# Performance work log

Measured on AMD Instinct MI355X. Metric: run time of the kernel, lower is better.

Reference implementation:

```python
import jax, jax.numpy as jnp
import numpy as np

N = 4096
IN_F = 256
OUT_F = 64
HEADS = 8
ALPHA = 0.2  # LeakyReLU negative slope


def setup_inputs() -> dict:
    key = jax.random.key(0)
    k1, k2, k3, k4 = jax.random.split(key, 4)
    X = jax.random.normal(k1, (N, IN_F), dtype=jnp.float32)
    adj = jax.random.randint(k2, (N, N), 0, 2, dtype=jnp.int32)
    # self-loops so every row has at least one neighbor (softmax well-defined)
    idx = jnp.arange(N)
    adj = adj.at[idx, idx].set(1)
    W = jax.random.normal(k3, (HEADS, IN_F, OUT_F), dtype=jnp.float32) * 0.05
    a = jax.random.normal(k4, (HEADS, 2 * OUT_F, 1), dtype=jnp.float32) * 0.05
    return {"X": X, "adj": adj, "W": W, "a": a}


def reference(X, adj, W, a):
    # H: [heads, N, F]
    H = jnp.einsum('ni,hio->hno', X, W)
    F_ = H.shape[-1]
    # cat([h_i, h_j]) @ a  ==  h_i @ a[:F] + h_j @ a[F:]
    a1 = a[:, :F_, 0]   # [heads, F]
    a2 = a[:, F_:, 0]   # [heads, F]
    f1 = jnp.einsum('hnf,hf->hn', H, a1)  # score contribution of row node i
    f2 = jnp.einsum('hnf,hf->hn', H, a2)  # score contribution of col node j
    e = jax.nn.leaky_relu(f1[:, :, None] + f2[:, None, :], negative_slope=ALPHA)  # [heads, N, N]
    e = jnp.where(adj[None, :, :] == 0, -jnp.inf, e)
    attention = jax.nn.softmax(e, axis=-1)
    # dropout omitted (eval mode)
    H_out = jnp.einsum('hnm,hmf->hnf', attention, H)  # [heads, N, F]
    return H_out.mean(axis=0)  # [N, F]
```

## Files before the change

kernel.cpp:

```cpp
#include <hip/hip_runtime.h>
#include <hip/hip_bf16.h>

#define N_NODES 4096
#define IN_F 256
#define OUT_F 64
#define HEADS 8
#define ALPHA 0.2f

typedef _Float16 f16x8 __attribute__((ext_vector_type(8)));
typedef float f32x4 __attribute__((ext_vector_type(4)));
union U4 { uint4 u; f16x8 h; unsigned w[4]; };

#define WFRAG_OFF 0
#define BFRAG_OFF (WFRAG_OFF + 8*8*4*64*8*2)
#define F1_OFF    (BFRAG_OFF + 8*128*4*64*8*2)
#define GP_OFF    (F1_OFF + 8*4096*4)
#define GN_OFF    (GP_OFF + 8*4096*2)
#define ADJ_OFF   (GN_OFF + 8*4096*2)

static __device__ __forceinline__ unsigned pkmul(unsigned a, unsigned b) {
  unsigned r; asm("v_pk_mul_f16 %0, %1, %2" : "=v"(r) : "v"(a), "v"(b)); return r;
}
static __device__ __forceinline__ unsigned pkmax(unsigned a, unsigned b) {
  unsigned r; asm("v_pk_max_f16 %0, %1, %2" : "=v"(r) : "v"(a), "v"(b)); return r;
}
static __device__ __forceinline__ unsigned short f2h_bits(float f) {
  return __builtin_bit_cast(unsigned short, (_Float16)f);
}

__global__ __launch_bounds__(256) void k_pre(const float* __restrict__ W,
                                             _Float16* __restrict__ wfrag,
                                             float* __restrict__ out) {
  int b = blockIdx.x, t = threadIdx.x;
  if (b < 8) {
    int h = b;
    for (int pos = t; pos < 2048; pos += 256) {
      int kt = pos >> 8, ct = (pos >> 6) & 3, l = pos & 63;
      int lr = l & 15, lg = l >> 4;
#pragma unroll
      for (int e = 0; e < 8; ++e)
        wfrag[(size_t)(((h*8 + kt)*4 + ct)*64 + l) * 8 + e]
          = (_Float16)W[(size_t)(h*256 + kt*32 + lg*8 + e) * 64 + ct*16 + lr];
    }
  } else {
    float4* oz = ((float4*)out) + (size_t)(b - 8) * 8192;
    float4 zz = make_float4(0.f, 0.f, 0.f, 0.f);
    for (int q = t; q < 8192; q += 256) oz[q] = zz;
  }
}

__global__ __launch_bounds__(256) void k_main(
    const float* __restrict__ X, const int* __restrict__ adj,
    const _Float16* __restrict__ wfrag, const float* __restrict__ a,
    unsigned long long* __restrict__ bits, _Float16* __restrict__ bfrag,
    float* __restrict__ f1, _Float16* __restrict__ Gp, _Float16* __restrict__ Gn) {
  int b = blockIdx.x, t = threadIdx.x;
  if (b >= 512) {
    int b2 = b - 512;
    int lane = t & 63;
    int waveid = b2 * 4 + (t >> 6);
#pragma unroll
    for (int it2 = 0; it2 < 8; ++it2) {
      int w0 = waveid + (it2*4 + 0) * 8192;
      int w1 = waveid + (it2*4 + 1) * 8192;
      int w2 = waveid + (it2*4 + 2) * 8192;
      int w3 = waveid + (it2*4 + 3) * 8192;
      int v0 = __builtin_nontemporal_load(adj + (size_t)w0 * 64 + lane);
      int v1 = __builtin_nontemporal_load(adj + (size_t)w1 * 64 + lane);
      int v2 = __builtin_nontemporal_load(adj + (size_t)w2 * 64 + lane);
      int v3 = __builtin_nontemporal_load(adj + (size_t)w3 * 64 + lane);
      unsigned long long m0 = __ballot(v0 != 0);
      unsigned long long m1 = __ballot(v1 != 0);
      unsigned long long m2 = __ballot(v2 != 0);
      unsigned long long m3 = __ballot(v3 != 0);
      if (lane == 0) { bits[w0] = m0; bits[w1] = m1; bits[w2] = m2; bits[w3] = m3; }
    }
    return;
  }
  int h = b & 7, rb = b >> 3;
  int w = t >> 6, l = t & 63;
  int i0 = rb * 64 + w * 16;
  int r = l & 15, g = l >> 4;
  const U4* wv = (const U4*)wfrag;
  f32x4 z = {0.f, 0.f, 0.f, 0.f};
  f32x4 acc[4] = {z, z, z, z};
#pragma unroll
  for (int kt = 0; kt < 8; ++kt) {
    const float4* xr = (const float4*)(X + (size_t)(i0 + r) * 256 + (kt*4 + g) * 8);
    float4 x0 = xr[0], x1 = xr[1];
    U4 af;
    af.h[0] = (_Float16)x0.x; af.h[1] = (_Float16)x0.y;
    af.h[2] = (_Float16)x0.z; af.h[3] = (_Float16)x0.w;
    af.h[4] = (_Float16)x1.x; af.h[5] = (_Float16)x1.y;
    af.h[6] = (_Float16)x1.z; af.h[7] = (_Float16)x1.w;
#pragma unroll
    for (int ct = 0; ct < 4; ++ct) {
      U4 bv = wv[((h*8 + kt)*4 + ct)*64 + l];
      acc[ct] = __builtin_amdgcn_mfma_f32_16x16x32_f16(af.h, bv.h, acc[ct], 0, 0, 0);
    }
  }
  int jb = i0 + g*4;
#pragma unroll
  for (int ct = 0; ct < 4; ++ct) {
    size_t base = ((((size_t)h*128 + (jb>>5))*4 + ct)*64 + ((jb>>3)&3)*16 + r) * 8
                  + (jb & 7);
    union { short4 s; _Float16 hh[4]; } sv;
#pragma unroll
    for (int ri = 0; ri < 4; ++ri) sv.hh[ri] = (_Float16)acc[ct][ri];
    *(short4*)(bfrag + base) = sv.s;
  }
  float a1v[4], a2v[4];
#pragma unroll
  for (int ct = 0; ct < 4; ++ct) {
    a1v[ct] = a[h*128 + ct*16 + r];
    a2v[ct] = a[h*128 + 64 + ct*16 + r];
  }
#pragma unroll
  for (int ri = 0; ri < 4; ++ri) {
    float s1 = acc[0][ri]*a1v[0] + acc[1][ri]*a1v[1]
             + acc[2][ri]*a1v[2] + acc[3][ri]*a1v[3];
    float s2 = acc[0][ri]*a2v[0] + acc[1][ri]*a2v[1]
             + acc[2][ri]*a2v[2] + acc[3][ri]*a2v[3];
#pragma unroll
    for (int off = 1; off < 16; off <<= 1) {
      s1 += __shfl_xor(s1, off);
      s2 += __shfl_xor(s2, off);
    }
    if (r == 0) {
      int row = i0 + g*4 + ri;
      f1[h*4096 + row] = s1;
      Gp[h*4096 + row] = (_Float16)__expf(s2);
      Gn[h*4096 + row] = (_Float16)__expf(ALPHA * s2);
    }
  }
}

#define ATTN_BODY(PF, JT, DOPF) {                                              \
  U4 gp, gn;                                                                   \
  gp.u = Gs0[(JT)*4 + g].u;                                                    \
  gn.u = Gs1[(JT)*4 + g].u;                                                    \
  U4 b0, b1, b2, b3;                                                           \
  b0.u = PF[0]; b1.u = PF[1]; b2.u = PF[2]; b3.u = PF[3];                      \
  _Pragma("unroll")                                                            \
  for (int rg = 0; rg < 2; ++rg) {                                             \
    unsigned wm = Lb[rh32 + rg*16 + r][JT];                                    \
    U4 av;                                                                     \
    _Pragma("unroll")                                                          \
    for (int p = 0; p < 4; ++p) {                                              \
      unsigned pm = pkmax(pkmul(Epp[rg], gp.w[p]), pkmul(Enn[rg], gn.w[p]));   \
      av.w[p] = pm & MLUT[(wm >> (g8 + 2*p)) & 3u];                            \
    }                                                                          \
    acc[rg][0] = __builtin_amdgcn_mfma_f32_16x16x32_f16(av.h, b0.h, acc[rg][0], 0,0,0); \
    acc[rg][1] = __builtin_amdgcn_mfma_f32_16x16x32_f16(av.h, b1.h, acc[rg][1], 0,0,0); \
    acc[rg][2] = __builtin_amdgcn_mfma_f32_16x16x32_f16(av.h, b2.h, acc[rg][2], 0,0,0); \
    acc[rg][3] = __builtin_amdgcn_mfma_f32_16x16x32_f16(av.h, b3.h, acc[rg][3], 0,0,0); \
    dn[rg]     = __builtin_amdgcn_mfma_f32_16x16x32_f16(av.h, bones.h, dn[rg], 0,0,0);  \
  }                                                                            \
  if (DOPF) {                                                                  \
    _Pragma("unroll")                                                          \
    for (int c = 0; c < 4; ++c) PF[c] = bfh[((JT) + 2)*256 + c*64];            \
  }                                                                            \
}

#define WRBUF(i) {                                                             \
  _Pragma("unroll")                                                            \
  for (int rg = 0; rg < 2; ++rg) {                                             \
    _Pragma("unroll")                                                          \
    for (int ct = 0; ct < 4; ++ct) redp[(i)*640 + (rg*4+ct)*64 + l] = acc[rg][ct]; \
    redp[(i)*640 + 512 + rg*64 + l] = dn[rg];                                  \
  } }
#define ADBUF(i) {                                                             \
  _Pragma("unroll")                                                            \
  for (int rg = 0; rg < 2; ++rg) {                                             \
    _Pragma("unroll")                                                          \
    for (int ct = 0; ct < 4; ++ct) acc[rg][ct] += redp[(i)*640 + (rg*4+ct)*64 + l]; \
    dn[rg] += redp[(i)*640 + 512 + rg*64 + l];                                 \
  } }

__global__ __launch_bounds__(512, 4) void k_attn(
    const float* __restrict__ f1, const unsigned int* __restrict__ adjbits,
    const _Float16* __restrict__ Gp, const _Float16* __restrict__ Gn,
    const _Float16* __restrict__ bfrag, float* __restrict__ out) {
  __shared__ __align__(16) char smem[49408];
  __shared__ unsigned MLUT[4];
  unsigned (*Lb)[129] = (unsigned(*)[129])smem;
  U4* Gs0 = (U4*)(smem + 33024);
  U4* Gs1 = (U4*)(smem + 41216);
  f32x4* redp = (f32x4*)smem;
  int b = blockIdx.x;
  int h = b & 7, rs = b >> 3;
  int i0 = rs * 64;
  int t = threadIdx.x, wid = t >> 6, l = t & 63;
  int rh = wid >> 2, jq = wid & 3;
  int rh32 = rh * 32;
  int r = l & 15, g = l >> 4, g8 = g * 8;
  if (t < 4) MLUT[t] = ((t & 1) ? 0xFFFFu : 0u) | ((t & 2) ? 0xFFFF0000u : 0u);
  const uint4* bfh = (const uint4*)bfrag + (size_t)h * 32768 + l;
  int jt0 = jq * 32;
  uint4 pA[4], pB[4];
#pragma unroll
  for (int c = 0; c < 4; ++c) pA[c] = bfh[jt0 * 256 + c*64];
#pragma unroll
  for (int c = 0; c < 4; ++c) pB[c] = bfh[(jt0 + 1) * 256 + c*64];
  for (int q = t; q < 8192; q += 512)
    Lb[q >> 7][q & 127] = adjbits[(size_t)(i0 + (q >> 7)) * 128 + (q & 127)];
  Gs0[t].u = ((const uint4*)(Gp + (size_t)h * 4096))[t];
  Gs1[t].u = ((const uint4*)(Gn + (size_t)h * 4096))[t];
  unsigned Epp[2], Enn[2];
#pragma unroll
  for (int rg = 0; rg < 2; ++rg) {
    float f1r = f1[h * N_NODES + i0 + rh32 + rg*16 + r];
    unsigned short ep = f2h_bits(__expf(f1r));
    unsigned short en = f2h_bits(__expf(ALPHA * f1r));
    Epp[rg] = ep | ((unsigned)ep << 16);
    Enn[rg] = en | ((unsigned)en << 16);
  }
  unsigned ov = (r == 0) ? 0x3C003C00u : 0u;
  U4 bones; bones.u = make_uint4(ov, ov, ov, ov);
  __syncthreads();
  f32x4 z = {0.f,0.f,0.f,0.f};
  f32x4 acc[2][4] = {{z,z,z,z},{z,z,z,z}};
  f32x4 dn[2] = {z, z};
  for (int q2 = 0; q2 < 16; ++q2) {
    ATTN_BODY(pA, jt0 + q2*2,     (q2 < 15));
    ATTN_BODY(pB, jt0 + q2*2 + 1, (q2 < 15));
  }
  __syncthreads();
  if (jq == 1 || jq == 3) WRBUF(rh*2 + (jq >> 1));
  __syncthreads();
  if (jq == 0) ADBUF(rh*2);
  if (jq == 2) ADBUF(rh*2 + 1);
  __syncthreads();
  if (jq == 2) WRBUF(rh);
  __syncthreads();
  if (jq == 0) {
    ADBUF(rh);
#pragma unroll
    for (int rg = 0; rg < 2; ++rg)
#pragma unroll
      for (int ri = 0; ri < 4; ++ri) {
        float dr = __shfl(dn[rg][ri], l & 48);
        float sc = 0.125f / dr;
        float* op = out + (size_t)(i0 + rh32 + rg*16 + g*4 + ri) * 64;
        atomicAdd(op + r,      acc[rg][0][ri] * sc);
        atomicAdd(op + 16 + r, acc[rg][1][ri] * sc);
        atomicAdd(op + 32 + r, acc[rg][2][ri] * sc);
        atomicAdd(op + 48 + r, acc[rg][3][ri] * sc);
      }
  }
}

extern "C" void kernel_launch(void* const* d_in, const int* in_sizes, int n_in,
                              void* d_out, int out_size, void* d_ws, size_t ws_size,
                              hipStream_t stream) {
  const float* X = (const float*)d_in[0];
  const int* adj = (const int*)d_in[1];
  const float* W = (const float*)d_in[2];
  const float* a = (const float*)d_in[3];
  float* out = (float*)d_out;
  char* ws = (char*)d_ws;

  _Float16* wfrag = (_Float16*)(ws + WFRAG_OFF);
  _Float16* bfrag = (_Float16*)(ws + BFRAG_OFF);
  float* f1 = (float*)(ws + F1_OFF);
  _Float16* Gp = (_Float16*)(ws + GP_OFF);
  _Float16* Gn = (_Float16*)(ws + GN_OFF);
  unsigned long long* bits64 = (unsigned long long*)(ws + ADJ_OFF);
  const unsigned int* bits32 = (const unsigned int*)(ws + ADJ_OFF);

  k_pre<<<dim3(16), dim3(256), 0, stream>>>(W, wfrag, out);
  k_main<<<dim3(2560), dim3(256), 0, stream>>>(X, adj, wfrag, a, bits64, bfrag,
                                               f1, Gp, Gn);
  k_attn<<<dim3(512), dim3(512), 0, stream>>>(f1, bits32, Gp, Gn, bfrag, out);
}
```

Measured before the change: 71.93 us.

## Read adjacency bits and G vectors from global, compute masks with bit ops

The attention kernel stops staging adjacency bitmasks and Gp/Gn into shared memory. Each lane now loads its mask words and G vectors directly from global memory (cache) inside the loop, and the pre-loop barrier is removed. The LDS lookup-table mask is replaced by a v_bfi_b32 plus packed arithmetic shift sequence, and the prep kernel reorders its blocks so the bit-packing blocks come first. This aims to remove the staging latency and LDS traffic and to shrink shared memory for better occupancy, but the inner loop now carries global-load latency.

```diff
diff --git a/kernel.cpp b/kernel.cpp
--- a/kernel.cpp
+++ b/kernel.cpp
@@ -55,10 +55,9 @@
     unsigned long long* __restrict__ bits, _Float16* __restrict__ bfrag,
     float* __restrict__ f1, _Float16* __restrict__ Gp, _Float16* __restrict__ Gn) {
   int b = blockIdx.x, t = threadIdx.x;
-  if (b >= 512) {
-    int b2 = b - 512;
+  if (b < 2048) {
     int lane = t & 63;
-    int waveid = b2 * 4 + (t >> 6);
+    int waveid = b * 4 + (t >> 6);
 #pragma unroll
     for (int it2 = 0; it2 < 8; ++it2) {
       int w0 = waveid + (it2*4 + 0) * 8192;
@@ -77,7 +76,8 @@
     }
     return;
   }
-  int h = b & 7, rb = b >> 3;
+  int b2 = b - 2048;
+  int h = b2 & 7, rb = b2 >> 3;
   int w = t >> 6, l = t & 63;
   int i0 = rb * 64 + w * 16;
   int r = l & 15, g = l >> 4;
@@ -135,20 +135,30 @@
   }
 }
 
-#define ATTN_BODY(PF, JT, DOPF) {                                              \
+#define MASKW(wmg, p, dst) {                                                   \
+  unsigned t1 = (wmg) << (15 - 2*(p));                                         \
+  unsigned t2 = (wmg) << (30 - 2*(p));                                         \
+  unsigned tw;                                                                 \
+  asm("v_bfi_b32 %0, %1, %2, %3" : "=v"(tw) : "v"(lowsel), "v"(t1), "v"(t2));  \
+  asm("v_pk_ashrrev_i16 %0, %1, %2" : "=v"(dst) : "v"(sh15), "v"(tw));         \
+}
+
+#define ATTN_BODY(PF, JT, WM0, WM1, DOPF) {                                    \
   U4 gp, gn;                                                                   \
-  gp.u = Gs0[(JT)*4 + g].u;                                                    \
-  gn.u = Gs1[(JT)*4 + g].u;                                                    \
+  gp.u = gpb[(JT)*4];                                                          \
+  gn.u = gnb[(JT)*4];                                                          \
   U4 b0, b1, b2, b3;                                                           \
   b0.u = PF[0]; b1.u = PF[1]; b2.u = PF[2]; b3.u = PF[3];                      \
+  unsigned wmg0 = (WM0) >> g8, wmg1 = (WM1) >> g8;                             \
   _Pragma("unroll")                                                            \
   for (int rg = 0; rg < 2; ++rg) {                                             \
-    unsigned wm = Lb[rh32 + rg*16 + r][JT];                                    \
+    unsigned wmg = rg ? wmg1 : wmg0;                                           \
     U4 av;                                                                     \
     _Pragma("unroll")                                                          \
     for (int p = 0; p < 4; ++p) {                                              \
       unsigned pm = pkmax(pkmul(Epp[rg], gp.w[p]), pkmul(Enn[rg], gn.w[p]));   \
-      av.w[p] = pm & MLUT[(wm >> (g8 + 2*p)) & 3u];                            \
+      unsigned m; MASKW(wmg, p, m);                                            \
+      av.w[p] = pm & m;                                                        \
     }                                                                          \
     acc[rg][0] = __builtin_amdgcn_mfma_f32_16x16x32_f16(av.h, b0.h, acc[rg][0], 0,0,0); \
     acc[rg][1] = __builtin_amdgcn_mfma_f32_16x16x32_f16(av.h, b1.h, acc[rg][1], 0,0,0); \
@@ -181,12 +191,7 @@
     const float* __restrict__ f1, const unsigned int* __restrict__ adjbits,
     const _Float16* __restrict__ Gp, const _Float16* __restrict__ Gn,
     const _Float16* __restrict__ bfrag, float* __restrict__ out) {
-  __shared__ __align__(16) char smem[49408];
-  __shared__ unsigned MLUT[4];
-  unsigned (*Lb)[129] = (unsigned(*)[129])smem;
-  U4* Gs0 = (U4*)(smem + 33024);
-  U4* Gs1 = (U4*)(smem + 41216);
-  f32x4* redp = (f32x4*)smem;
+  __shared__ f32x4 redp[2560];
   int b = blockIdx.x;
   int h = b & 7, rs = b >> 3;
   int i0 = rs * 64;
@@ -194,18 +199,18 @@
   int rh = wid >> 2, jq = wid & 3;
   int rh32 = rh * 32;
   int r = l & 15, g = l >> 4, g8 = g * 8;
-  if (t < 4) MLUT[t] = ((t & 1) ? 0xFFFFu : 0u) | ((t & 2) ? 0xFFFF0000u : 0u);
+  unsigned lowsel = 0x0000FFFFu, sh15 = 0x000F000Fu;
   const uint4* bfh = (const uint4*)bfrag + (size_t)h * 32768 + l;
+  const uint4* gpb = (const uint4*)(Gp + (size_t)h * 4096) + g;
+  const uint4* gnb = (const uint4*)(Gn + (size_t)h * 4096) + g;
+  const unsigned* lb0 = adjbits + (size_t)(i0 + rh32 + r) * 128;
+  const unsigned* lb1 = lb0 + 16 * 128;
   int jt0 = jq * 32;
   uint4 pA[4], pB[4];
 #pragma unroll
   for (int c = 0; c < 4; ++c) pA[c] = bfh[jt0 * 256 + c*64];
 #pragma unroll
   for (int c = 0; c < 4; ++c) pB[c] = bfh[(jt0 + 1) * 256 + c*64];
-  for (int q = t; q < 8192; q += 512)
-    Lb[q >> 7][q & 127] = adjbits[(size_t)(i0 + (q >> 7)) * 128 + (q & 127)];
-  Gs0[t].u = ((const uint4*)(Gp + (size_t)h * 4096))[t];
-  Gs1[t].u = ((const uint4*)(Gn + (size_t)h * 4096))[t];
   unsigned Epp[2], Enn[2];
 #pragma unroll
   for (int rg = 0; rg < 2; ++rg) {
@@ -217,13 +222,15 @@
   }
   unsigned ov = (r == 0) ? 0x3C003C00u : 0u;
   U4 bones; bones.u = make_uint4(ov, ov, ov, ov);
-  __syncthreads();
   f32x4 z = {0.f,0.f,0.f,0.f};
   f32x4 acc[2][4] = {{z,z,z,z},{z,z,z,z}};
   f32x4 dn[2] = {z, z};
   for (int q2 = 0; q2 < 16; ++q2) {
-    ATTN_BODY(pA, jt0 + q2*2,     (q2 < 15));
-    ATTN_BODY(pB, jt0 + q2*2 + 1, (q2 < 15));
+    int jt = jt0 + q2 * 2;
+    uint2 wmp0 = *(const uint2*)(lb0 + jt);
+    uint2 wmp1 = *(const uint2*)(lb1 + jt);
+    ATTN_BODY(pA, jt,     wmp0.x, wmp1.x, (q2 < 15));
+    ATTN_BODY(pB, jt + 1, wmp0.y, wmp1.y, (q2 < 15));
   }
   __syncthreads();
   if (jq == 1 || jq == 3) WRBUF(rh*2 + (jq >> 1));
```

Result: slower. 86.81 us (+20.7%).
